# Kernel optimization log

Measured on AMD Instinct MI355X. Metric: run time of the kernel, lower is better.

Reference implementation:

```python
import jax, jax.numpy as jnp
import numpy as np

N = 100000
E = 1600000
IN_DIM = 128
HEADS = 4
OUT_DIM = 32


def setup_inputs() -> dict:
    key = jax.random.key(0)
    k1, k2, k3, k4, k5 = jax.random.split(key, 5)
    x = jax.random.normal(k1, (N, IN_DIM), dtype=jnp.float32)
    edge_index = jax.random.randint(k2, (2, E), 0, N, dtype=jnp.int64)
    # torch Linear weight: (out_features, in_features) = (HEADS*OUT_DIM, IN_DIM)
    W = jax.random.normal(k3, (HEADS * OUT_DIM, IN_DIM), dtype=jnp.float32) * 0.05
    a_src = jax.random.normal(k4, (HEADS, OUT_DIM), dtype=jnp.float32)
    a_dst = jax.random.normal(k5, (HEADS, OUT_DIM), dtype=jnp.float32)
    return {"x": x, "edge_index": edge_index, "W": W, "a_src": a_src, "a_dst": a_dst}


def reference(x, edge_index, W, a_src, a_dst):
    n = x.shape[0]
    H, D = a_src.shape
    # h: (N, H, D)
    h = (x @ W.T).reshape(n, H, D)
    src, dst = edge_index[0], edge_index[1]
    # per-edge attention logits: (E, H)
    e_src = jnp.einsum('ehd,hd->eh', h[src], a_src)
    e_dst = jnp.einsum('ehd,hd->eh', h[dst], a_dst)
    e = jax.nn.leaky_relu(e_src + e_dst, negative_slope=0.2)
    # segment max per destination node (init zeros, include_self=True as in torch)
    e_max = jnp.zeros((n, H), dtype=x.dtype).at[dst].max(e)
    e_exp = jnp.exp(e - e_max[dst])
    e_sum = jnp.zeros((n, H), dtype=x.dtype).at[dst].add(e_exp)
    alpha = e_exp / (e_sum[dst] + 1e-8)  # (E, H)
    # weighted messages and scatter-add aggregation
    msg = h[src] * alpha[..., None]  # (E, H, D)
    out = jnp.zeros((n, H, D), dtype=x.dtype).at[dst].add(msg)
    return out.reshape(n, H * D)  # concat=True
```

## Files before the change

kernel.cpp:

```cpp
#include <hip/hip_runtime.h>

#define IN_DIM 128
#define HD 128
#define HEADS 4
#define MD 64
#define CAP 128
#define NCOHORT 8

typedef int   ni4  __attribute__((ext_vector_type(4)));
typedef float nf4  __attribute__((ext_vector_type(4)));
typedef unsigned short nu4 __attribute__((ext_vector_type(4)));

__device__ __forceinline__ float lrelu(float v){ return v > 0.f ? v : 0.2f*v; }
__device__ __forceinline__ float4 add4(float4 a, float4 b){
  return make_float4(a.x+b.x, a.y+b.y, a.z+b.z, a.w+b.w);
}
__device__ __forceinline__ float4 expl4(float4 v){
  return make_float4(__expf(lrelu(v.x)), __expf(lrelu(v.y)), __expf(lrelu(v.z)), __expf(lrelu(v.w)));
}
__device__ __forceinline__ unsigned short f2b(float f){
  unsigned u = __float_as_uint(f);
  return (unsigned short)((u + 0x7FFFu + ((u >> 16) & 1u)) >> 16);
}
__device__ __forceinline__ float b2f(unsigned short b){
  return __uint_as_float(((unsigned)b) << 16);
}
__device__ __forceinline__ float blo(unsigned u){ return __uint_as_float(u << 16); }
__device__ __forceinline__ float bhi(unsigned u){ return __uint_as_float(u & 0xFFFF0000u); }

__global__ __launch_bounds__(256) void k_init(const float* __restrict__ W, float* __restrict__ WT,
                                              int* __restrict__ count, int n_nodes){
  int idx = blockIdx.x*256 + threadIdx.x;
  if (idx < 128*128){ int j = idx >> 7, k = idx & 127; WT[k*128 + j] = W[idx]; }
  for (int n = idx; n < n_nodes; n += gridDim.x*256) count[n] = 0;
}

__global__ __launch_bounds__(256) void k_gemm_scatter(
    const float* __restrict__ x, const float* __restrict__ WT,
    const float* __restrict__ a_src, const float* __restrict__ a_dst,
    unsigned short* __restrict__ h, float* __restrict__ s, float* __restrict__ t,
    const int* __restrict__ esrc, const int* __restrict__ edst, int E_,
    int* __restrict__ count, int* __restrict__ slots,
    int n_nodes, int sc_blocks, int R){
  __shared__ float xs[32][132];
  const int tid = threadIdx.x;

  if ((int)blockIdx.x < sc_blocks){
    const unsigned c = blockIdx.x & (NCOHORT-1);
    const int gth = ((int)blockIdx.x >> 3)*256 + tid;
    const int gstride = (sc_blocks >> 3)*256;
    const unsigned lo = c*(unsigned)R;

#define PROC(D, S) { unsigned d_ = (unsigned)(D); \
    if (d_ - lo < (unsigned)R){ \
      int pos = atomicAdd(&count[d_], 1); \
      if (pos < MD) slots[(size_t)d_*MD + pos] = (S); } }

    const bool al16 = ((((size_t)edst) | ((size_t)esrc)) & 15) == 0;
    int done = 0;
    if (al16){
      const int ngrp = E_ >> 3;
      const ni4* dst4 = (const ni4*)edst;
      const ni4* src4 = (const ni4*)esrc;
      for (int g8 = gth; g8 < ngrp; g8 += gstride){
        ni4 d0 = __builtin_nontemporal_load(&dst4[2*g8]);
        ni4 d1 = __builtin_nontemporal_load(&dst4[2*g8+1]);
        ni4 s0 = __builtin_nontemporal_load(&src4[2*g8]);
        ni4 s1 = __builtin_nontemporal_load(&src4[2*g8+1]);
        PROC(d0.x, s0.x); PROC(d0.y, s0.y); PROC(d0.z, s0.z); PROC(d0.w, s0.w);
        PROC(d1.x, s1.x); PROC(d1.y, s1.y); PROC(d1.z, s1.z); PROC(d1.w, s1.w);
      }
      done = ngrp << 3;
    }
    for (int e = done + gth; e < E_; e += gstride){
      int dv = __builtin_nontemporal_load(&edst[e]);
      int sv = __builtin_nontemporal_load(&esrc[e]);
      PROC(dv, sv);
    }
#undef PROC
  } else {
    const int tile = blockIdx.x - sc_blocks;
    const int base = tile*32;
    if (base >= n_nodes) return;
    const int jg  = tid & 31;
    const int ng  = tid >> 5;
    const int j4  = jg*4;
    const float4 as4 = *(const float4*)(a_src + j4);
    const float4 ad4 = *(const float4*)(a_dst + j4);

    for (int i = tid; i < 32*32; i += 256){
      int row = i >> 5, c4 = (i & 31)*4;
      nf4 v = {0.f,0.f,0.f,0.f};
      if (base + row < n_nodes)
        v = __builtin_nontemporal_load((const nf4*)(x + (size_t)(base+row)*IN_DIM + c4));
      *(nf4*)&xs[row][c4] = v;
    }
    __syncthreads();

    float acc[4][4];
    #pragma unroll
    for (int i=0;i<4;++i){ acc[i][0]=acc[i][1]=acc[i][2]=acc[i][3]=0.f; }
    const int nb = ng*4;
    const float* wp = WT + j4;

    float4 wc0 = *(const float4*)(wp);
    float4 wc1 = *(const float4*)(wp + 128);
    float4 wc2 = *(const float4*)(wp + 256);
    float4 wc3 = *(const float4*)(wp + 384);
    for (int k=0;k<128;k+=4){
      const float* wq = wp + (size_t)(((k+4) & 127))*128;
      float4 wn0 = *(const float4*)(wq);
      float4 wn1 = *(const float4*)(wq + 128);
      float4 wn2 = *(const float4*)(wq + 256);
      float4 wn3 = *(const float4*)(wq + 384);
      #pragma unroll
      for (int u=0;u<4;++u){
        float4 xv = *(const float4*)&xs[nb+u][k];
        acc[u][0] = fmaf(wc0.x, xv.x, acc[u][0]);
        acc[u][1] = fmaf(wc0.y, xv.x, acc[u][1]);
        acc[u][2] = fmaf(wc0.z, xv.x, acc[u][2]);
        acc[u][3] = fmaf(wc0.w, xv.x, acc[u][3]);
        acc[u][0] = fmaf(wc1.x, xv.y, acc[u][0]);
        acc[u][1] = fmaf(wc1.y, xv.y, acc[u][1]);
        acc[u][2] = fmaf(wc1.z, xv.y, acc[u][2]);
        acc[u][3] = fmaf(wc1.w, xv.y, acc[u][3]);
        acc[u][0] = fmaf(wc2.x, xv.z, acc[u][0]);
        acc[u][1] = fmaf(wc2.y, xv.z, acc[u][1]);
        acc[u][2] = fmaf(wc2.z, xv.z, acc[u][2]);
        acc[u][3] = fmaf(wc2.w, xv.z, acc[u][3]);
        acc[u][0] = fmaf(wc3.x, xv.w, acc[u][0]);
        acc[u][1] = fmaf(wc3.y, xv.w, acc[u][1]);
        acc[u][2] = fmaf(wc3.z, xv.w, acc[u][2]);
        acc[u][3] = fmaf(wc3.w, xv.w, acc[u][3]);
      }
      wc0 = wn0; wc1 = wn1; wc2 = wn2; wc3 = wn3;
    }

    #pragma unroll
    for (int i=0;i<4;++i){
      int node = base + nb + i;
      if (node < n_nodes){
        nu4 hv = { f2b(acc[i][0]), f2b(acc[i][1]), f2b(acc[i][2]), f2b(acc[i][3]) };
        __builtin_nontemporal_store(hv, (nu4*)(h + (size_t)node*HD + j4));
      }
    }
    #pragma unroll
    for (int i=0;i<4;++i){
      float ps = acc[i][0]*as4.x + acc[i][1]*as4.y + acc[i][2]*as4.z + acc[i][3]*as4.w;
      float pt = acc[i][0]*ad4.x + acc[i][1]*ad4.y + acc[i][2]*ad4.z + acc[i][3]*ad4.w;
      ps += __shfl_xor(ps,1,64); ps += __shfl_xor(ps,2,64); ps += __shfl_xor(ps,4,64);
      pt += __shfl_xor(pt,1,64); pt += __shfl_xor(pt,2,64); pt += __shfl_xor(pt,4,64);
      if ((jg & 7) == 0){
        int node = base + nb + i;
        if (node < n_nodes){
          int hh = jg >> 3;
          s[node*HEADS + hh] = ps;
          t[node*HEADS + hh] = pt;
        }
      }
    }
  }
}

__global__ __launch_bounds__(256) void k_aggregate2(const int* __restrict__ slots,
    const int* __restrict__ count, const unsigned short* __restrict__ h,
    const float* __restrict__ s, const float* __restrict__ t,
    float* __restrict__ out, int n_nodes){
  __shared__ int   s_src[4][MD];
  __shared__ float s_exp[4][MD][4];
  const int lane = threadIdx.x & 63;
  const int slot = threadIdx.x >> 6;
  const int n = blockIdx.x*4 + slot;
  if (n >= n_nodes) return;
  int cnt = count[n]; if (cnt > MD) cnt = MD;
  const float4 t4 = *(const float4*)(t + n*HEADS);

  float4 z4 = make_float4(0.f,0.f,0.f,0.f);
  if (lane < cnt){
    int src = __builtin_nontemporal_load(&slots[(size_t)n*MD + lane]);
    s_src[slot][lane] = src;
    float4 s4 = *(const float4*)(s + src*HEADS);
    float4 e4 = expl4(add4(s4, t4));
    z4 = e4;
    *(float4*)&s_exp[slot][lane][0] = e4;
  }
  #pragma unroll
  for (int o=1;o<64;o<<=1){
    z4.x += __shfl_xor(z4.x,o,64);
    z4.y += __shfl_xor(z4.y,o,64);
    z4.z += __shfl_xor(z4.z,o,64);
    z4.w += __shfl_xor(z4.w,o,64);
  }

  const int qtr = lane >> 4;
  const int q   = lane & 15;
  const int hd  = q >> 2;
  float zh = hd==0 ? z4.x : hd==1 ? z4.y : hd==2 ? z4.z : z4.w;
  const float r = 1.f/(zh + 1e-8f);
  float4 accA = make_float4(0.f,0.f,0.f,0.f);
  float4 accB = make_float4(0.f,0.f,0.f,0.f);
  const unsigned short* hq = h + 8*q;

#define FMA8(U, W) \
  accA.x = fmaf(W, blo(U.x), accA.x); accA.y = fmaf(W, bhi(U.x), accA.y); \
  accA.z = fmaf(W, blo(U.y), accA.z); accA.w = fmaf(W, bhi(U.y), accA.w); \
  accB.x = fmaf(W, blo(U.z), accB.x); accB.y = fmaf(W, bhi(U.z), accB.y); \
  accB.z = fmaf(W, blo(U.w), accB.z); accB.w = fmaf(W, bhi(U.w), accB.w);

  int i = 0;
  for (; i + 8 <= cnt; i += 8){
    int eA = i + qtr, eB = i + 4 + qtr;
    int aA = s_src[slot][eA], aB = s_src[slot][eB];
    uint4 uA = *(const uint4*)(hq + (size_t)aA*HD);
    uint4 uB = *(const uint4*)(hq + (size_t)aB*HD);
    float wA = s_exp[slot][eA][hd], wB = s_exp[slot][eB][hd];
    FMA8(uA, wA); FMA8(uB, wB);
  }
  if (i + 4 <= cnt){
    int eA = i + qtr;
    int aA = s_src[slot][eA];
    uint4 uA = *(const uint4*)(hq + (size_t)aA*HD);
    float wA = s_exp[slot][eA][hd];
    FMA8(uA, wA);
    i += 4;
  }
  if (i < cnt && qtr < cnt - i){
    int eA = i + qtr;
    int aA = s_src[slot][eA];
    uint4 uA = *(const uint4*)(hq + (size_t)aA*HD);
    float wA = s_exp[slot][eA][hd];
    FMA8(uA, wA);
  }
#undef FMA8

  #pragma unroll
  for (int o=16;o<64;o<<=1){
    accA.x += __shfl_xor(accA.x,o,64); accA.y += __shfl_xor(accA.y,o,64);
    accA.z += __shfl_xor(accA.z,o,64); accA.w += __shfl_xor(accA.w,o,64);
    accB.x += __shfl_xor(accB.x,o,64); accB.y += __shfl_xor(accB.y,o,64);
    accB.z += __shfl_xor(accB.z,o,64); accB.w += __shfl_xor(accB.w,o,64);
  }
  if (qtr == 0){
    *(float4*)(out + (size_t)n*HD + 8*q)     = make_float4(accA.x*r, accA.y*r, accA.z*r, accA.w*r);
    *(float4*)(out + (size_t)n*HD + 8*q + 4) = make_float4(accB.x*r, accB.y*r, accB.z*r, accB.w*r);
  }
}

__global__ __launch_bounds__(256) void k_transpose_w(const float* __restrict__ W, float* __restrict__ WT){
  int idx = blockIdx.x*256 + threadIdx.x;
  int j = idx >> 7, k = idx & 127;
  WT[k*128 + j] = W[idx];
}

__global__ __launch_bounds__(256) void k_gemm(const float* __restrict__ x, const float* __restrict__ WT,
    const float* __restrict__ a_src, const float* __restrict__ a_dst,
    unsigned short* __restrict__ h, float* __restrict__ s, float* __restrict__ t,
    int n_nodes, int n_tiles){
  __shared__ float xs[64][132];
  const int tid = threadIdx.x;
  const int jg  = tid & 31;
  const int ng  = tid >> 5;
  const int j4  = jg*4;
  const float4 as4 = *(const float4*)(a_src + j4);
  const float4 ad4 = *(const float4*)(a_dst + j4);

  for (int tile = blockIdx.x; tile < n_tiles; tile += gridDim.x){
    const int base = tile*64;
    __syncthreads();
    for (int i = tid; i < 64*32; i += 256){
      int row = i >> 5, c4 = (i & 31)*4;
      float4 v = make_float4(0.f,0.f,0.f,0.f);
      if (base + row < n_nodes) v = *(const float4*)(x + (size_t)(base+row)*IN_DIM + c4);
      *(float4*)&xs[row][c4] = v;
    }
    __syncthreads();

    float acc[8][4];
    #pragma unroll
    for (int i=0;i<8;++i){ acc[i][0]=acc[i][1]=acc[i][2]=acc[i][3]=0.f; }
    const int nb = ng*8;
    for (int k=0;k<128;k+=4){
      float4 w0 = *(const float4*)(WT + (k  )*128 + j4);
      float4 w1 = *(const float4*)(WT + (k+1)*128 + j4);
      float4 w2 = *(const float4*)(WT + (k+2)*128 + j4);
      float4 w3 = *(const float4*)(WT + (k+3)*128 + j4);
      #pragma unroll
      for (int i=0;i<8;++i){
        float4 xv = *(const float4*)&xs[nb+i][k];
        acc[i][0] = fmaf(w0.x, xv.x, acc[i][0]); acc[i][1] = fmaf(w0.y, xv.x, acc[i][1]);
        acc[i][2] = fmaf(w0.z, xv.x, acc[i][2]); acc[i][3] = fmaf(w0.w, xv.x, acc[i][3]);
        acc[i][0] = fmaf(w1.x, xv.y, acc[i][0]); acc[i][1] = fmaf(w1.y, xv.y, acc[i][1]);
        acc[i][2] = fmaf(w1.z, xv.y, acc[i][2]); acc[i][3] = fmaf(w1.w, xv.y, acc[i][3]);
        acc[i][0] = fmaf(w2.x, xv.z, acc[i][0]); acc[i][1] = fmaf(w2.y, xv.z, acc[i][1]);
        acc[i][2] = fmaf(w2.z, xv.z, acc[i][2]); acc[i][3] = fmaf(w2.w, xv.z, acc[i][3]);
        acc[i][0] = fmaf(w3.x, xv.w, acc[i][0]); acc[i][1] = fmaf(w3.y, xv.w, acc[i][1]);
        acc[i][2] = fmaf(w3.z, xv.w, acc[i][2]); acc[i][3] = fmaf(w3.w, xv.w, acc[i][3]);
      }
    }
    #pragma unroll
    for (int i=0;i<8;++i){
      int node = base + nb + i;
      if (node < n_nodes)
        *(ushort4*)(h + (size_t)node*HD + j4) =
          make_ushort4(f2b(acc[i][0]), f2b(acc[i][1]), f2b(acc[i][2]), f2b(acc[i][3]));
    }
    #pragma unroll
    for (int i=0;i<8;++i){
      float ps = acc[i][0]*as4.x + acc[i][1]*as4.y + acc[i][2]*as4.z + acc[i][3]*as4.w;
      float pt = acc[i][0]*ad4.x + acc[i][1]*ad4.y + acc[i][2]*ad4.z + acc[i][3]*ad4.w;
      ps += __shfl_xor(ps,1,64); ps += __shfl_xor(ps,2,64); ps += __shfl_xor(ps,4,64);
      pt += __shfl_xor(pt,1,64); pt += __shfl_xor(pt,2,64); pt += __shfl_xor(pt,4,64);
      if ((jg & 7) == 0){
        int node = base + nb + i;
        if (node < n_nodes){
          int hh = jg >> 3;
          s[node*HEADS + hh] = ps;
          t[node*HEADS + hh] = pt;
        }
      }
    }
  }
}

__global__ __launch_bounds__(256) void k_hist(const int* __restrict__ dst, int E_,
                                              int* __restrict__ count, int R){
  const int c  = blockIdx.x & (NCOHORT-1);
  const int g  = (blockIdx.x >> 3)*256 + threadIdx.x;
  const int gs = (gridDim.x >> 3)*256;
  const unsigned lo = (unsigned)(c*R);
  for (int e = g; e < E_; e += gs){
    unsigned d = (unsigned)dst[e];
    if (d - lo < (unsigned)R) atomicAdd(&count[d], 1);
  }
}

__global__ void k_offsets(const int* __restrict__ count, int n_nodes,
                          int* __restrict__ offs, int* __restrict__ wcur, int* __restrict__ cursor){
  int n = blockIdx.x*blockDim.x + threadIdx.x;
  int lane = threadIdx.x & 63;
  int c = (n < n_nodes) ? count[n] : 0;
  int incl = c;
  #pragma unroll
  for (int o=1;o<64;o<<=1){
    int v = __shfl_up(incl, o, 64);
    if (lane >= o) incl += v;
  }
  int wave_total = __shfl(incl, 63, 64);
  int base = 0;
  if (lane == 63) base = atomicAdd(cursor, wave_total);
  base = __shfl(base, 63, 64);
  if (n < n_nodes){
    int off = base + incl - c;
    offs[n] = off; wcur[n] = off;
  }
}

__global__ __launch_bounds__(256) void k_scatter(const int* __restrict__ src, const int* __restrict__ dst,
                                                 int E_, int* __restrict__ wcur,
                                                 int* __restrict__ csr_src, int R){
  const int c  = blockIdx.x & (NCOHORT-1);
  const int g  = (blockIdx.x >> 3)*256 + threadIdx.x;
  const int gs = (gridDim.x >> 3)*256;
  const unsigned lo = (unsigned)(c*R);
  for (int e = g; e < E_; e += gs){
    unsigned d = (unsigned)dst[e];
    if (d - lo < (unsigned)R){
      int pos = atomicAdd(&wcur[d], 1);
      csr_src[pos] = src[e];
    }
  }
}

__global__ __launch_bounds__(256) void k_aggregate(const int* __restrict__ csr_src,
    const int* __restrict__ offs, const int* __restrict__ count,
    const unsigned short* __restrict__ h, const float* __restrict__ s, const float* __restrict__ t,
    float* __restrict__ out, int n_nodes){
  __shared__ int   s_src[4][CAP];
  __shared__ float s_exp[4][CAP][4];
  const int lane = threadIdx.x & 63;
  const int slot = threadIdx.x >> 6;
  const int n = blockIdx.x*4 + slot;
  if (n >= n_nodes) return;
  const int start = offs[n];
  const int cnt   = count[n];
  const float4 t4 = *(const float4*)(t + n*HEADS);
  const bool fast = (cnt <= CAP);

  float4 z4 = make_float4(0.f,0.f,0.f,0.f);
  if (fast){
    #pragma unroll
    for (int j=0;j<2;++j){
      int i = lane + j*64;
      if (i < cnt){
        int src = csr_src[start+i];
        s_src[slot][i] = src;
        float4 s4 = *(const float4*)(s + src*HEADS);
        float4 e4 = expl4(add4(s4, t4));
        z4 = add4(z4, e4);
        *(float4*)&s_exp[slot][i][0] = e4;
      }
    }
  } else {
    for (int i = lane; i < cnt; i += 64){
      int src = csr_src[start+i];
      float4 s4 = *(const float4*)(s + src*HEADS);
      z4 = add4(z4, expl4(add4(s4, t4)));
    }
  }
  #pragma unroll
  for (int o=1;o<64;o<<=1){
    z4.x += __shfl_xor(z4.x,o,64);
    z4.y += __shfl_xor(z4.y,o,64);
    z4.z += __shfl_xor(z4.z,o,64);
    z4.w += __shfl_xor(z4.w,o,64);
  }

  if (fast){
    const int half = lane >> 5;
    const int fl   = lane & 31;
    const int hd   = fl >> 3;
    float zh = hd==0 ? z4.x : hd==1 ? z4.y : hd==2 ? z4.z : z4.w;
    const float r = 1.f/(zh + 1e-8f);
    float4 acc = make_float4(0.f,0.f,0.f,0.f);
    int i = 0;
    for (; i + 4 <= cnt; i += 4){
      int a0 = s_src[slot][i+half], a1 = s_src[slot][i+2+half];
      ushort4 u0 = *(const ushort4*)(h + (size_t)a0*HD + 4*fl);
      ushort4 u1 = *(const ushort4*)(h + (size_t)a1*HD + 4*fl);
      float e0 = s_exp[slot][i+half][hd], e1 = s_exp[slot][i+2+half][hd];
      acc.x = fmaf(e0, b2f(u0.x), acc.x); acc.y = fmaf(e0, b2f(u0.y), acc.y);
      acc.z = fmaf(e0, b2f(u0.z), acc.z); acc.w = fmaf(e0, b2f(u0.w), acc.w);
      acc.x = fmaf(e1, b2f(u1.x), acc.x); acc.y = fmaf(e1, b2f(u1.y), acc.y);
      acc.z = fmaf(e1, b2f(u1.z), acc.z); acc.w = fmaf(e1, b2f(u1.w), acc.w);
    }
    if (i + 2 <= cnt){
      int a0 = s_src[slot][i+half];
      ushort4 u0 = *(const ushort4*)(h + (size_t)a0*HD + 4*fl);
      float e0 = s_exp[slot][i+half][hd];
      acc.x = fmaf(e0, b2f(u0.x), acc.x); acc.y = fmaf(e0, b2f(u0.y), acc.y);
      acc.z = fmaf(e0, b2f(u0.z), acc.z); acc.w = fmaf(e0, b2f(u0.w), acc.w);
      i += 2;
    }
    if (i < cnt && half == 0){
      int a0 = s_src[slot][i];
      ushort4 u0 = *(const ushort4*)(h + (size_t)a0*HD + 4*fl);
      float e0 = s_exp[slot][i][hd];
      acc.x = fmaf(e0, b2f(u0.x), acc.x); acc.y = fmaf(e0, b2f(u0.y), acc.y);
      acc.z = fmaf(e0, b2f(u0.z), acc.z); acc.w = fmaf(e0, b2f(u0.w), acc.w);
    }
    acc.x += __shfl_xor(acc.x, 32, 64);
    acc.y += __shfl_xor(acc.y, 32, 64);
    acc.z += __shfl_xor(acc.z, 32, 64);
    acc.w += __shfl_xor(acc.w, 32, 64);
    if (half == 0){
      *(float4*)(out + (size_t)n*HD + 4*fl) = make_float4(acc.x*r, acc.y*r, acc.z*r, acc.w*r);
    }
  } else {
    const int hd = lane >> 4;
    float zh = hd==0 ? z4.x : hd==1 ? z4.y : hd==2 ? z4.z : z4.w;
    const float r = 1.f/(zh + 1e-8f);
    float th = hd==0 ? t4.x : hd==1 ? t4.y : hd==2 ? t4.z : t4.w;
    float2 acc = make_float2(0.f,0.f);
    for (int i = 0; i < cnt; ++i){
      int src = csr_src[start+i];
      float4 s4 = *(const float4*)(s + src*HEADS);
      float sh = hd==0 ? s4.x : hd==1 ? s4.y : hd==2 ? s4.z : s4.w;
      float e = __expf(lrelu(sh+th));
      ushort2 u = *(const ushort2*)(h + (size_t)src*HD + 2*lane);
      acc.x = fmaf(e, b2f(u.x), acc.x); acc.y = fmaf(e, b2f(u.y), acc.y);
    }
    *(float2*)(out + (size_t)n*HD + 2*lane) = make_float2(acc.x*r, acc.y*r);
  }
}

extern "C" void kernel_launch(void* const* d_in, const int* in_sizes, int n_in,
                              void* d_out, int out_size, void* d_ws, size_t ws_size,
                              hipStream_t stream) {
  const float* x     = (const float*)d_in[0];
  const int*   ei    = (const int*)d_in[1];
  const float* W     = (const float*)d_in[2];
  const float* a_src = (const float*)d_in[3];
  const float* a_dst = (const float*)d_in[4];
  float* out = (float*)d_out;

  const int n_nodes = in_sizes[0] / IN_DIM;
  const int E_      = in_sizes[1] / 2;
  const int R       = (n_nodes + NCOHORT - 1) / NCOHORT;

  char* ws = (char*)d_ws;
  size_t off = 0;
  auto alloc = [&](size_t bytes){ size_t cur = off; off += (bytes + 255) & ~255ULL; return cur; };

  float*          WT    = (float*)(ws + alloc(128*128*4));
  unsigned short* h     = (unsigned short*)(ws + alloc((size_t)n_nodes*HD*2));
  float*          s     = (float*)(ws + alloc((size_t)n_nodes*HEADS*4));
  float*          t     = (float*)(ws + alloc((size_t)n_nodes*HEADS*4));
  int*            count = (int*)  (ws + alloc((size_t)n_nodes*4));

  size_t slotted_need = off + (((size_t)n_nodes*MD*4 + 255) & ~255ULL);

  if (ws_size >= slotted_need){
    int* slots = (int*)(ws + alloc((size_t)n_nodes*MD*4));

    int init_grid = (n_nodes + 255)/256; if (init_grid < 64) init_grid = 64;
    k_init<<<init_grid, 256, 0, stream>>>(W, WT, count, n_nodes);

    const int n_tiles32 = (n_nodes + 31) / 32;
    const int sc_blocks = 2048;
    k_gemm_scatter<<<sc_blocks + n_tiles32, 256, 0, stream>>>(
        x, WT, a_src, a_dst, h, s, t, ei, ei + E_, E_,
        count, slots, n_nodes, sc_blocks, R);

    k_aggregate2<<<(n_nodes+3)/4, 256, 0, stream>>>(slots, count, h, s, t, out, n_nodes);
  } else {
    const int n_tiles = (n_nodes + 63) / 64;
    int* offs    = (int*)(ws + alloc((size_t)n_nodes*4));
    int* wcur    = (int*)(ws + alloc((size_t)n_nodes*4));
    int* cursor  = (int*)(ws + alloc(4));
    int* csr_src = (int*)(ws + alloc((size_t)E_*4));

    hipMemsetAsync(count, 0, (size_t)n_nodes*4, stream);
    hipMemsetAsync(cursor, 0, 4, stream);
    k_transpose_w<<<64, 256, 0, stream>>>(W, WT);
    k_gemm<<<n_tiles, 256, 0, stream>>>(x, WT, a_src, a_dst, h, s, t, n_nodes, n_tiles);
    k_hist<<<2048, 256, 0, stream>>>(ei + E_, E_, count, R);
    k_offsets<<<(n_nodes+255)/256, 256, 0, stream>>>(count, n_nodes, offs, wcur, cursor);
    k_scatter<<<2048, 256, 0, stream>>>(ei, ei + E_, E_, wcur, csr_src, R);
    k_aggregate<<<(n_nodes+3)/4, 256, 0, stream>>>(csr_src, offs, count, h, s, t, out, n_nodes);
  }
}
```

Baseline: 210.7 us.

## Replace global-atomic slot scatter with two-level bucket sort via shared-memory histograms

Replaces the fused GEMM+scatter kernel, which did global atomicAdd per edge into per-node slot lists, with a separate GEMM kernel and a multi-pass bucket sort. Edges are binned by dst>>8 with per-chunk shared histograms, a column scan, a bucket-base scan and a scatter into a bucket buffer. Then one block per bucket builds per-node slots using shared-memory atomics. This removes contended global atomics and random global slot writes, at the cost of more kernel launches, extra passes over the edge list and losing the overlap between the GEMM and the scatter.

```diff
diff --git a/kernel.cpp b/kernel.cpp
--- a/kernel.cpp
+++ b/kernel.cpp
@@ -6,8 +6,9 @@
 #define MD 64
 #define CAP 128
 #define NCOHORT 8
-
-typedef int   ni4  __attribute__((ext_vector_type(4)));
+#define CHUNK 2048
+#define NBMAX 512
+
 typedef float nf4  __attribute__((ext_vector_type(4)));
 typedef unsigned short nu4 __attribute__((ext_vector_type(4)));
 
@@ -28,137 +29,189 @@
 __device__ __forceinline__ float blo(unsigned u){ return __uint_as_float(u << 16); }
 __device__ __forceinline__ float bhi(unsigned u){ return __uint_as_float(u & 0xFFFF0000u); }
 
-__global__ __launch_bounds__(256) void k_init(const float* __restrict__ W, float* __restrict__ WT,
-                                              int* __restrict__ count, int n_nodes){
+__global__ __launch_bounds__(256) void k_init(const float* __restrict__ W, float* __restrict__ WT){
   int idx = blockIdx.x*256 + threadIdx.x;
-  if (idx < 128*128){ int j = idx >> 7, k = idx & 127; WT[k*128 + j] = W[idx]; }
-  for (int n = idx; n < n_nodes; n += gridDim.x*256) count[n] = 0;
-}
-
-__global__ __launch_bounds__(256) void k_gemm_scatter(
+  int j = idx >> 7, k = idx & 127;
+  WT[k*128 + j] = W[idx];
+}
+
+__global__ __launch_bounds__(256) void k_gemm_only(
     const float* __restrict__ x, const float* __restrict__ WT,
     const float* __restrict__ a_src, const float* __restrict__ a_dst,
     unsigned short* __restrict__ h, float* __restrict__ s, float* __restrict__ t,
-    const int* __restrict__ esrc, const int* __restrict__ edst, int E_,
-    int* __restrict__ count, int* __restrict__ slots,
-    int n_nodes, int sc_blocks, int R){
+    int n_nodes){
   __shared__ float xs[32][132];
   const int tid = threadIdx.x;
-
-  if ((int)blockIdx.x < sc_blocks){
-    const unsigned c = blockIdx.x & (NCOHORT-1);
-    const int gth = ((int)blockIdx.x >> 3)*256 + tid;
-    const int gstride = (sc_blocks >> 3)*256;
-    const unsigned lo = c*(unsigned)R;
-
-#define PROC(D, S) { unsigned d_ = (unsigned)(D); \
-    if (d_ - lo < (unsigned)R){ \
-      int pos = atomicAdd(&count[d_], 1); \
-      if (pos < MD) slots[(size_t)d_*MD + pos] = (S); } }
-
-    const bool al16 = ((((size_t)edst) | ((size_t)esrc)) & 15) == 0;
-    int done = 0;
-    if (al16){
-      const int ngrp = E_ >> 3;
-      const ni4* dst4 = (const ni4*)edst;
-      const ni4* src4 = (const ni4*)esrc;
-      for (int g8 = gth; g8 < ngrp; g8 += gstride){
-        ni4 d0 = __builtin_nontemporal_load(&dst4[2*g8]);
-        ni4 d1 = __builtin_nontemporal_load(&dst4[2*g8+1]);
-        ni4 s0 = __builtin_nontemporal_load(&src4[2*g8]);
-        ni4 s1 = __builtin_nontemporal_load(&src4[2*g8+1]);
-        PROC(d0.x, s0.x); PROC(d0.y, s0.y); PROC(d0.z, s0.z); PROC(d0.w, s0.w);
-        PROC(d1.x, s1.x); PROC(d1.y, s1.y); PROC(d1.z, s1.z); PROC(d1.w, s1.w);
-      }
-      done = ngrp << 3;
-    }
-    for (int e = done + gth; e < E_; e += gstride){
-      int dv = __builtin_nontemporal_load(&edst[e]);
-      int sv = __builtin_nontemporal_load(&esrc[e]);
-      PROC(dv, sv);
-    }
-#undef PROC
-  } else {
-    const int tile = blockIdx.x - sc_blocks;
-    const int base = tile*32;
-    if (base >= n_nodes) return;
-    const int jg  = tid & 31;
-    const int ng  = tid >> 5;
-    const int j4  = jg*4;
-    const float4 as4 = *(const float4*)(a_src + j4);
-    const float4 ad4 = *(const float4*)(a_dst + j4);
-
-    for (int i = tid; i < 32*32; i += 256){
-      int row = i >> 5, c4 = (i & 31)*4;
-      nf4 v = {0.f,0.f,0.f,0.f};
-      if (base + row < n_nodes)
-        v = __builtin_nontemporal_load((const nf4*)(x + (size_t)(base+row)*IN_DIM + c4));
-      *(nf4*)&xs[row][c4] = v;
-    }
-    __syncthreads();
-
-    float acc[4][4];
-    #pragma unroll
-    for (int i=0;i<4;++i){ acc[i][0]=acc[i][1]=acc[i][2]=acc[i][3]=0.f; }
-    const int nb = ng*4;
-    const float* wp = WT + j4;
-
-    float4 wc0 = *(const float4*)(wp);
-    float4 wc1 = *(const float4*)(wp + 128);
-    float4 wc2 = *(const float4*)(wp + 256);
-    float4 wc3 = *(const float4*)(wp + 384);
-    for (int k=0;k<128;k+=4){
-      const float* wq = wp + (size_t)(((k+4) & 127))*128;
-      float4 wn0 = *(const float4*)(wq);
-      float4 wn1 = *(const float4*)(wq + 128);
-      float4 wn2 = *(const float4*)(wq + 256);
-      float4 wn3 = *(const float4*)(wq + 384);
-      #pragma unroll
-      for (int u=0;u<4;++u){
-        float4 xv = *(const float4*)&xs[nb+u][k];
-        acc[u][0] = fmaf(wc0.x, xv.x, acc[u][0]);
-        acc[u][1] = fmaf(wc0.y, xv.x, acc[u][1]);
-        acc[u][2] = fmaf(wc0.z, xv.x, acc[u][2]);
-        acc[u][3] = fmaf(wc0.w, xv.x, acc[u][3]);
-        acc[u][0] = fmaf(wc1.x, xv.y, acc[u][0]);
-        acc[u][1] = fmaf(wc1.y, xv.y, acc[u][1]);
-        acc[u][2] = fmaf(wc1.z, xv.y, acc[u][2]);
-        acc[u][3] = fmaf(wc1.w, xv.y, acc[u][3]);
-        acc[u][0] = fmaf(wc2.x, xv.z, acc[u][0]);
-        acc[u][1] = fmaf(wc2.y, xv.z, acc[u][1]);
-        acc[u][2] = fmaf(wc2.z, xv.z, acc[u][2]);
-        acc[u][3] = fmaf(wc2.w, xv.z, acc[u][3]);
-        acc[u][0] = fmaf(wc3.x, xv.w, acc[u][0]);
-        acc[u][1] = fmaf(wc3.y, xv.w, acc[u][1]);
-        acc[u][2] = fmaf(wc3.z, xv.w, acc[u][2]);
-        acc[u][3] = fmaf(wc3.w, xv.w, acc[u][3]);
-      }
-      wc0 = wn0; wc1 = wn1; wc2 = wn2; wc3 = wn3;
-    }
-
-    #pragma unroll
-    for (int i=0;i<4;++i){
+  const int base = blockIdx.x*32;
+  if (base >= n_nodes) return;
+  const int jg  = tid & 31;
+  const int ng  = tid >> 5;
+  const int j4  = jg*4;
+  const float4 as4 = *(const float4*)(a_src + j4);
+  const float4 ad4 = *(const float4*)(a_dst + j4);
+
+  for (int i = tid; i < 32*32; i += 256){
+    int row = i >> 5, c4 = (i & 31)*4;
+    nf4 v = {0.f,0.f,0.f,0.f};
+    if (base + row < n_nodes)
+      v = __builtin_nontemporal_load((const nf4*)(x + (size_t)(base+row)*IN_DIM + c4));
+    *(nf4*)&xs[row][c4] = v;
+  }
+  __syncthreads();
+
+  float acc[4][4];
+  #pragma unroll
+  for (int i=0;i<4;++i){ acc[i][0]=acc[i][1]=acc[i][2]=acc[i][3]=0.f; }
+  const int nb = ng*4;
+  const float* wp = WT + j4;
+
+  float4 wc0 = *(const float4*)(wp);
+  float4 wc1 = *(const float4*)(wp + 128);
+  float4 wc2 = *(const float4*)(wp + 256);
+  float4 wc3 = *(const float4*)(wp + 384);
+  for (int k=0;k<128;k+=4){
+    const float* wq = wp + (size_t)(((k+4) & 127))*128;
+    float4 wn0 = *(const float4*)(wq);
+    float4 wn1 = *(const float4*)(wq + 128);
+    float4 wn2 = *(const float4*)(wq + 256);
+    float4 wn3 = *(const float4*)(wq + 384);
+    #pragma unroll
+    for (int u=0;u<4;++u){
+      float4 xv = *(const float4*)&xs[nb+u][k];
+      acc[u][0] = fmaf(wc0.x, xv.x, acc[u][0]);
+      acc[u][1] = fmaf(wc0.y, xv.x, acc[u][1]);
+      acc[u][2] = fmaf(wc0.z, xv.x, acc[u][2]);
+      acc[u][3] = fmaf(wc0.w, xv.x, acc[u][3]);
+      acc[u][0] = fmaf(wc1.x, xv.y, acc[u][0]);
+      acc[u][1] = fmaf(wc1.y, xv.y, acc[u][1]);
+      acc[u][2] = fmaf(wc1.z, xv.y, acc[u][2]);
+      acc[u][3] = fmaf(wc1.w, xv.y, acc[u][3]);
+      acc[u][0] = fmaf(wc2.x, xv.z, acc[u][0]);
+      acc[u][1] = fmaf(wc2.y, xv.z, acc[u][1]);
+      acc[u][2] = fmaf(wc2.z, xv.z, acc[u][2]);
+      acc[u][3] = fmaf(wc2.w, xv.z, acc[u][3]);
+      acc[u][0] = fmaf(wc3.x, xv.w, acc[u][0]);
+      acc[u][1] = fmaf(wc3.y, xv.w, acc[u][1]);
+      acc[u][2] = fmaf(wc3.z, xv.w, acc[u][2]);
+      acc[u][3] = fmaf(wc3.w, xv.w, acc[u][3]);
+    }
+    wc0 = wn0; wc1 = wn1; wc2 = wn2; wc3 = wn3;
+  }
+
+  #pragma unroll
+  for (int i=0;i<4;++i){
+    int node = base + nb + i;
+    if (node < n_nodes){
+      nu4 hv = { f2b(acc[i][0]), f2b(acc[i][1]), f2b(acc[i][2]), f2b(acc[i][3]) };
+      __builtin_nontemporal_store(hv, (nu4*)(h + (size_t)node*HD + j4));
+    }
+  }
+  #pragma unroll
+  for (int i=0;i<4;++i){
+    float ps = acc[i][0]*as4.x + acc[i][1]*as4.y + acc[i][2]*as4.z + acc[i][3]*as4.w;
+    float pt = acc[i][0]*ad4.x + acc[i][1]*ad4.y + acc[i][2]*ad4.z + acc[i][3]*ad4.w;
+    ps += __shfl_xor(ps,1,64); ps += __shfl_xor(ps,2,64); ps += __shfl_xor(ps,4,64);
+    pt += __shfl_xor(pt,1,64); pt += __shfl_xor(pt,2,64); pt += __shfl_xor(pt,4,64);
+    if ((jg & 7) == 0){
       int node = base + nb + i;
       if (node < n_nodes){
-        nu4 hv = { f2b(acc[i][0]), f2b(acc[i][1]), f2b(acc[i][2]), f2b(acc[i][3]) };
-        __builtin_nontemporal_store(hv, (nu4*)(h + (size_t)node*HD + j4));
+        int hh = jg >> 3;
+        s[node*HEADS + hh] = ps;
+        t[node*HEADS + hh] = pt;
       }
     }
-    #pragma unroll
-    for (int i=0;i<4;++i){
-      float ps = acc[i][0]*as4.x + acc[i][1]*as4.y + acc[i][2]*as4.z + acc[i][3]*as4.w;
-      float pt = acc[i][0]*ad4.x + acc[i][1]*ad4.y + acc[i][2]*ad4.z + acc[i][3]*ad4.w;
-      ps += __shfl_xor(ps,1,64); ps += __shfl_xor(ps,2,64); ps += __shfl_xor(ps,4,64);
-      pt += __shfl_xor(pt,1,64); pt += __shfl_xor(pt,2,64); pt += __shfl_xor(pt,4,64);
-      if ((jg & 7) == 0){
-        int node = base + nb + i;
-        if (node < n_nodes){
-          int hh = jg >> 3;
-          s[node*HEADS + hh] = ps;
-          t[node*HEADS + hh] = pt;
-        }
-      }
-    }
+  }
+}
+
+__global__ __launch_bounds__(256) void k_bcount(const int* __restrict__ edst, int E_,
+                                                int* __restrict__ cmat, int NB){
+  __shared__ int hist[NBMAX];
+  const int tid = threadIdx.x;
+  for (int b = tid; b < NB; b += 256) hist[b] = 0;
+  __syncthreads();
+  const int base = blockIdx.x*CHUNK;
+  const int lim  = (base + CHUNK < E_) ? base + CHUNK : E_;
+  for (int i = base + tid; i < lim; i += 256)
+    atomicAdd(&hist[((unsigned)edst[i]) >> 8], 1);
+  __syncthreads();
+  for (int b = tid; b < NB; b += 256)
+    cmat[(size_t)blockIdx.x*NB + b] = hist[b];
+}
+
+__global__ __launch_bounds__(256) void k_bscan(int* __restrict__ cmat, int NCH, int NB,
+                                               int* __restrict__ btot){
+  const int lane = threadIdx.x & 63;
+  const int b = blockIdx.x*4 + (threadIdx.x >> 6);
+  if (b >= NB) return;
+  int run = 0;
+  for (int c0 = 0; c0 < NCH; c0 += 64){
+    int c = c0 + lane;
+    int v = (c < NCH) ? cmat[(size_t)c*NB + b] : 0;
+    int incl = v;
+    #pragma unroll
+    for (int o=1;o<64;o<<=1){ int u = __shfl_up(incl, o, 64); if (lane >= o) incl += u; }
+    if (c < NCH) cmat[(size_t)c*NB + b] = run + incl - v;
+    run += __shfl(incl, 63, 64);
+  }
+  if (lane == 0) btot[b] = run;
+}
+
+__global__ __launch_bounds__(64) void k_bbase(const int* __restrict__ btot, int NB,
+                                              int* __restrict__ bbase){
+  const int lane = threadIdx.x;
+  int run = 0;
+  for (int c0 = 0; c0 < NB; c0 += 64){
+    int c = c0 + lane;
+    int v = (c < NB) ? btot[c] : 0;
+    int incl = v;
+    #pragma unroll
+    for (int o=1;o<64;o<<=1){ int u = __shfl_up(incl, o, 64); if (lane >= o) incl += u; }
+    if (c < NB) bbase[c] = run + incl - v;
+    run += __shfl(incl, 63, 64);
+  }
+  if (lane == 0) bbase[NB] = run;
+}
+
+__global__ __launch_bounds__(256) void k_bscatter(const int* __restrict__ esrc,
+    const int* __restrict__ edst, int E_, const int* __restrict__ cmat,
+    const int* __restrict__ bbase, int* __restrict__ bucketbuf, int NB){
+  __shared__ int cur[NBMAX];
+  const int tid = threadIdx.x;
+  for (int b = tid; b < NB; b += 256)
+    cur[b] = bbase[b] + cmat[(size_t)blockIdx.x*NB + b];
+  __syncthreads();
+  const int base = blockIdx.x*CHUNK;
+  const int lim  = (base + CHUNK < E_) ? base + CHUNK : E_;
+  for (int i = base + tid; i < lim; i += 256){
+    unsigned d = (unsigned)edst[i];
+    int b = d >> 8;
+    int pos = atomicAdd(&cur[b], 1);
+    bucketbuf[pos] = esrc[i] | ((int)(d & 255u) << 24);
+  }
+}
+
+__global__ __launch_bounds__(256) void k_bslots(const int* __restrict__ bucketbuf,
+    const int* __restrict__ bbase, int* __restrict__ slots, int* __restrict__ count,
+    int n_nodes){
+  __shared__ int ncnt[256];
+  const int tid = threadIdx.x;
+  const int b = blockIdx.x;
+  const int lo = bbase[b], hi = bbase[b+1];
+  ncnt[tid] = 0;
+  __syncthreads();
+  for (int i = lo + tid; i < hi; i += 256)
+    atomicAdd(&ncnt[((unsigned)bucketbuf[i]) >> 24], 1);
+  __syncthreads();
+  int node = b*256 + tid;
+  if (node < n_nodes) count[node] = ncnt[tid];
+  __syncthreads();
+  ncnt[tid] = 0;
+  __syncthreads();
+  for (int i = lo + tid; i < hi; i += 256){
+    int p = bucketbuf[i];
+    int ld = ((unsigned)p) >> 24;
+    int pos = atomicAdd(&ncnt[ld], 1);
+    if (pos < MD) slots[(size_t)(b*256 + ld)*MD + pos] = p & 0xFFFFFF;
   }
 }
 
@@ -177,7 +230,7 @@
 
   float4 z4 = make_float4(0.f,0.f,0.f,0.f);
   if (lane < cnt){
-    int src = __builtin_nontemporal_load(&slots[(size_t)n*MD + lane]);
+    int src = slots[(size_t)n*MD + lane];
     s_src[slot][lane] = src;
     float4 s4 = *(const float4*)(s + src*HEADS);
     float4 e4 = expl4(add4(s4, t4));
@@ -244,12 +297,6 @@
     *(float4*)(out + (size_t)n*HD + 8*q)     = make_float4(accA.x*r, accA.y*r, accA.z*r, accA.w*r);
     *(float4*)(out + (size_t)n*HD + 8*q + 4) = make_float4(accB.x*r, accB.y*r, accB.z*r, accB.w*r);
   }
-}
-
-__global__ __launch_bounds__(256) void k_transpose_w(const float* __restrict__ W, float* __restrict__ WT){
-  int idx = blockIdx.x*256 + threadIdx.x;
-  int j = idx >> 7, k = idx & 127;
-  WT[k*128 + j] = W[idx];
 }
 
 __global__ __launch_bounds__(256) void k_gemm(const float* __restrict__ x, const float* __restrict__ WT,
@@ -486,42 +533,53 @@
   const int n_nodes = in_sizes[0] / IN_DIM;
   const int E_      = in_sizes[1] / 2;
   const int R       = (n_nodes + NCOHORT - 1) / NCOHORT;
+  const int NB      = (n_nodes + 255) >> 8;
+  const int NCH     = (E_ + CHUNK - 1) / CHUNK;
 
   char* ws = (char*)d_ws;
   size_t off = 0;
   auto alloc = [&](size_t bytes){ size_t cur = off; off += (bytes + 255) & ~255ULL; return cur; };
 
-  float*          WT    = (float*)(ws + alloc(128*128*4));
-  unsigned short* h     = (unsigned short*)(ws + alloc((size_t)n_nodes*HD*2));
-  float*          s     = (float*)(ws + alloc((size_t)n_nodes*HEADS*4));
-  float*          t     = (float*)(ws + alloc((size_t)n_nodes*HEADS*4));
-  int*            count = (int*)  (ws + alloc((size_t)n_nodes*4));
-
-  size_t slotted_need = off + (((size_t)n_nodes*MD*4 + 255) & ~255ULL);
-
-  if (ws_size >= slotted_need){
-    int* slots = (int*)(ws + alloc((size_t)n_nodes*MD*4));
-
-    int init_grid = (n_nodes + 255)/256; if (init_grid < 64) init_grid = 64;
-    k_init<<<init_grid, 256, 0, stream>>>(W, WT, count, n_nodes);
-
-    const int n_tiles32 = (n_nodes + 31) / 32;
-    const int sc_blocks = 2048;
-    k_gemm_scatter<<<sc_blocks + n_tiles32, 256, 0, stream>>>(
-        x, WT, a_src, a_dst, h, s, t, ei, ei + E_, E_,
-        count, slots, n_nodes, sc_blocks, R);
-
+  float*          WT = (float*)(ws + alloc(128*128*4));
+  unsigned short* h  = (unsigned short*)(ws + alloc((size_t)n_nodes*HD*2));
+  float*          s  = (float*)(ws + alloc((size_t)n_nodes*HEADS*4));
+  float*          t  = (float*)(ws + alloc((size_t)n_nodes*HEADS*4));
+
+  size_t ms_need = off
+    + (((size_t)n_nodes*4       + 255) & ~255ULL)
+    + (((size_t)n_nodes*MD*4    + 255) & ~255ULL)
+    + (((size_t)NCH*NB*4        + 255) & ~255ULL)
+    + (((size_t)NB*4            + 255) & ~255ULL)
+    + (((size_t)(NB+1)*4        + 255) & ~255ULL)
+    + (((size_t)E_*4            + 255) & ~255ULL);
+
+  if (ws_size >= ms_need && NB <= NBMAX && n_nodes < (1 << 24)){
+    int* count     = (int*)(ws + alloc((size_t)n_nodes*4));
+    int* slots     = (int*)(ws + alloc((size_t)n_nodes*MD*4));
+    int* cmat      = (int*)(ws + alloc((size_t)NCH*NB*4));
+    int* btot      = (int*)(ws + alloc((size_t)NB*4));
+    int* bbase     = (int*)(ws + alloc((size_t)(NB+1)*4));
+    int* bucketbuf = (int*)(ws + alloc((size_t)E_*4));
+
+    k_init<<<64, 256, 0, stream>>>(W, WT);
+    k_gemm_only<<<(n_nodes+31)/32, 256, 0, stream>>>(x, WT, a_src, a_dst, h, s, t, n_nodes);
+    k_bcount<<<NCH, 256, 0, stream>>>(ei + E_, E_, cmat, NB);
+    k_bscan<<<(NB+3)/4, 256, 0, stream>>>(cmat, NCH, NB, btot);
+    k_bbase<<<1, 64, 0, stream>>>(btot, NB, bbase);
+    k_bscatter<<<NCH, 256, 0, stream>>>(ei, ei + E_, E_, cmat, bbase, bucketbuf, NB);
+    k_bslots<<<NB, 256, 0, stream>>>(bucketbuf, bbase, slots, count, n_nodes);
     k_aggregate2<<<(n_nodes+3)/4, 256, 0, stream>>>(slots, count, h, s, t, out, n_nodes);
   } else {
-    const int n_tiles = (n_nodes + 63) / 64;
+    int* count   = (int*)(ws + alloc((size_t)n_nodes*4));
     int* offs    = (int*)(ws + alloc((size_t)n_nodes*4));
     int* wcur    = (int*)(ws + alloc((size_t)n_nodes*4));
     int* cursor  = (int*)(ws + alloc(4));
     int* csr_src = (int*)(ws + alloc((size_t)E_*4));
+    const int n_tiles = (n_nodes + 63) / 64;
 
     hipMemsetAsync(count, 0, (size_t)n_nodes*4, stream);
     hipMemsetAsync(cursor, 0, 4, stream);
-    k_transpose_w<<<64, 256, 0, stream>>>(W, WT);
+    k_init<<<64, 256, 0, stream>>>(W, WT);
     k_gemm<<<n_tiles, 256, 0, stream>>>(x, WT, a_src, a_dst, h, s, t, n_nodes, n_tiles);
     k_hist<<<2048, 256, 0, stream>>>(ei + E_, E_, count, R);
     k_offsets<<<(n_nodes+255)/256, 256, 0, stream>>>(count, n_nodes, offs, wcur, cursor);
```

Result: faster. 200.6 us (-4.8%).
